# Kernel optimization log

Measured on AMD Instinct MI355X. Metric: run time of the kernel, lower is better.

## Reference

```python
import jax, jax.numpy as jnp
import numpy as np


def _gru(x, Wih, Whh, bih, bhh):
    # single-layer torch-style GRU; x: [B,T,D] -> [B,T,H]
    H = Whh.shape[1]
    gi_all = jnp.einsum('btd,gd->btg', x, Wih) + bih  # [B,T,3H], input gates precomputed

    def step(h, gi):
        gh = h @ Whh.T + bhh
        ir, iz, inn = jnp.split(gi, 3, axis=-1)
        hr, hz, hn = jnp.split(gh, 3, axis=-1)
        r = jax.nn.sigmoid(ir + hr)
        zg = jax.nn.sigmoid(iz + hz)
        n = jnp.tanh(inn + r * hn)
        h_new = (1.0 - zg) * n + zg * h
        return h_new, h_new

    h0 = jnp.zeros((x.shape[0], H), x.dtype)
    _, hs = jax.lax.scan(step, h0, jnp.swapaxes(gi_all, 0, 1))
    return jnp.swapaxes(hs, 0, 1)


def _post(h, W1, b1, W2, b2):
    h = jax.nn.leaky_relu(h @ W1.T + b1, 0.1)
    return jax.nn.leaky_relu(h @ W2.T + b2, 0.1)


def setup_inputs() -> dict:
    B, T, X, Z, H, L = 512, 100, 38, 3, 500, 20
    key = jax.random.key(0)
    ks = iter(jax.random.split(key, 40))
    r = lambda shape, s=0.05: jax.random.normal(next(ks), shape, jnp.float32) * s
    return {
        'x': jax.random.normal(next(ks), (B, T, X), jnp.float32),
        'eps': jax.random.normal(next(ks), (B, T, Z), jnp.float32),
        'enc_Wih': r((3 * H, X)), 'enc_Whh': r((3 * H, H)), 'enc_bih': r((3 * H,)), 'enc_bhh': r((3 * H,)),
        'enc_W1': r((H, H)), 'enc_b1': r((H,)), 'enc_W2': r((H, H)), 'enc_b2': r((H,)),
        'zm_W': r((Z, H + Z)), 'zm_b': r((Z,)), 'zs_W': r((Z, H + Z)), 'zs_b': r((Z,)),
        'flow_w': r((L, Z), 0.5), 'flow_b': r((L,), 0.5), 'flow_u': r((L, Z), 0.5),
        'dec_Wih': r((3 * H, Z)), 'dec_Whh': r((3 * H, H)), 'dec_bih': r((3 * H,)), 'dec_bhh': r((3 * H,)),
        'dec_W1': r((H, H)), 'dec_b1': r((H,)), 'dec_W2': r((H, H)), 'dec_b2': r((H,)),
        'xm_W': r((X, H)), 'xm_b': r((X,)), 'xs_W': r((X, H)), 'xs_b': r((X,)),
    }


def reference(x, eps, enc_Wih, enc_Whh, enc_bih, enc_bhh, enc_W1, enc_b1, enc_W2, enc_b2,
              zm_W, zm_b, zs_W, zs_b, flow_w, flow_b, flow_u,
              dec_Wih, dec_Whh, dec_bih, dec_bhh, dec_W1, dec_b1, dec_W2, dec_b2,
              xm_W, xm_b, xs_W, xs_b):
    # ---- Encoder ----
    h = _gru(x, enc_Wih, enc_Whh, enc_bih, enc_bhh)
    h = _post(h, enc_W1, enc_b1, enc_W2, enc_b2)

    def lat_step(z_prev, inputs):
        ht, et = inputs
        inp = jnp.concatenate([ht, z_prev], axis=-1)
        mu = inp @ zm_W.T + zm_b
        std = jax.nn.softplus(inp @ zs_W.T + zs_b) + 1e-4
        zt = mu + std * et
        return zt, (zt, mu, std)

    z0 = jnp.zeros((x.shape[0], zm_W.shape[0]), x.dtype)
    _, (z_gen, z_mu, z_std) = jax.lax.scan(
        lat_step, z0, (jnp.swapaxes(h, 0, 1), jnp.swapaxes(eps, 0, 1)))
    z_gen = jnp.swapaxes(z_gen, 0, 1)
    z_mu = jnp.swapaxes(z_mu, 0, 1)
    z_std = jnp.swapaxes(z_std, 0, 1)

    # ---- Planar flow stack ----
    def flow_step(carry, p):
        z, ld = carry
        w, b, u = p
        wu = jnp.sum(w * u)
        m = -1.0 + jax.nn.softplus(wu)
        u_hat = u + (m - wu) * w / (jnp.sum(w * w) + 1e-7)
        lin = jnp.sum(z * w, axis=-1, keepdims=True) + b  # [B,T,1]
        t = jnp.tanh(lin)
        fz = z + u_hat * t
        det = 1.0 + (1.0 - t * t) * jnp.sum(u_hat * w)  # sum(u_hat*psi)
        ld = ld + jnp.log(jnp.abs(det) + 1e-7)
        return (fz, ld), None

    ld0 = jnp.zeros(z_gen.shape[:-1] + (1,), z_gen.dtype)
    (z_fin, log_det_jac), _ = jax.lax.scan(flow_step, (z_gen, ld0), (flow_w, flow_b, flow_u))

    # ---- Decoder ----
    hd = _gru(z_fin, dec_Wih, dec_Whh, dec_bih, dec_bhh)
    hd = _post(hd, dec_W1, dec_b1, dec_W2, dec_b2)
    x_rec_mu = hd @ xm_W.T + xm_b
    x_rec_std = jax.nn.softplus(hd @ xs_W.T + xs_b) + 1e-4
    return (x_rec_mu, x_rec_std, z_gen, z_fin, z_mu, z_std, log_det_jac)
```

## Files before the change

### kernel.cpp

```cpp
#include <hip/hip_runtime.h>

typedef unsigned short u16;
typedef unsigned int u32;
typedef unsigned long long u64;
typedef __bf16 bf16x8 __attribute__((ext_vector_type(8)));
typedef float f32x4 __attribute__((ext_vector_type(4)));
typedef u16 u16x8 __attribute__((ext_vector_type(8)));
typedef u16 u16x4 __attribute__((ext_vector_type(4)));
typedef u32 u32x4 __attribute__((ext_vector_type(4)));

#define MFMA16x16(a,b,c) __builtin_amdgcn_mfma_f32_16x16x32_bf16((a),(b),(c),0,0,0)

static __device__ __forceinline__ u16 f2bf(float f){
  u32 u = __builtin_bit_cast(u32, f);
  u += 0x7fffu + ((u >> 16) & 1u);
  return (u16)(u >> 16);
}
static __device__ __forceinline__ float bf2f(u16 h){
  u32 u = ((u32)h) << 16;
  return __builtin_bit_cast(float, u);
}
static __device__ __forceinline__ float fast_sigmoid(float x){
  return 1.f / (1.f + __expf(-x));
}
static __device__ __forceinline__ float fast_tanh(float x){
  float e = __expf(2.f * x);
  return 1.f - 2.f / (e + 1.f);
}
static __device__ __forceinline__ float fast_softplus(float x){
  return (x > 15.f) ? x : __logf(1.f + __expf(x));
}
static __device__ __forceinline__ f32x4 zero4(){
  f32x4 v; v[0]=0.f; v[1]=0.f; v[2]=0.f; v[3]=0.f; return v;
}

static __device__ __forceinline__ void build_one(
    u16* __restrict__ dst, int mode, int NT, int idx,
    const float* __restrict__ W0, const float* __restrict__ b0,
    const float* __restrict__ W1, const float* __restrict__ b1)
{
  int j    = idx & 7;
  int lane = (idx >> 3) & 63;
  int ntks = idx >> 9;
  int nt   = ntks % NT;
  int ks   = ntks / NT;
  int k    = ks * 32 + ((lane >> 4) << 3) + j;
  int ncol = (nt << 4) + (lane & 15);
  float v = 0.f;
  if (mode == 0){
    int g = ncol >> 9;
    int jin = ncol & 511;
    if (jin < 500){
      int row = g * 500 + jin;
      if (k < 500) v = W0[row * 500 + k];
      else if (k == 511) v = b0[row];
    }
  } else if (mode == 2){
    if (ncol < 500){
      if (k < 500) v = W0[ncol * 500 + k];
      else if (k == 511) v = b0[ncol];
    }
  } else if (mode == 3){
    int c = ncol;
    if (c < 3){
      if (k < 500) v = W0[c * 503 + k];
      else if (k == 511) v = b0[c];
    } else if (c < 6){
      int cc = c - 3;
      if (k < 500) v = W1[cc * 503 + k];
      else if (k == 511) v = b1[cc];
    }
  } else if (mode == 4){
    int grp = ncol / 48;
    int cc  = ncol - grp * 48;
    if (grp < 2 && cc < 38){
      const float* W  = grp ? W1 : W0;
      const float* bb = grp ? b1 : b0;
      if (k < 500) v = W[cc * 500 + k];
      else if (k == 511) v = bb[cc];
    }
  } else {
    int g = ncol >> 9;
    int jin = ncol & 511;
    if (jin < 500 && k < 38) v = W0[(g * 500 + jin) * 38 + k];
  }
  dst[idx] = f2bf(v);
}

__global__ void build_all(
    u16* ENCF, u16* DECF, u16* EGIF, u16* PF0, u16* PF1, u16* PF2, u16* PF3,
    u16* ZFR, u16* HFR, float* FPP, u32* CNT,
    const float* enc_Whh, const float* enc_bhh, const float* enc_Wih,
    const float* dec_Whh, const float* dec_bhh,
    const float* enc_W1, const float* enc_b1, const float* enc_W2, const float* enc_b2,
    const float* dec_W1, const float* dec_b1, const float* dec_W2, const float* dec_b2,
    const float* zm_W, const float* zm_b, const float* zs_W, const float* zs_b,
    const float* xm_W, const float* xm_b, const float* xs_W, const float* xs_b,
    const float* flow_w, const float* flow_b, const float* flow_u)
{
  const int b = blockIdx.x, tid = threadIdx.x;
  if      (b < 3072)  build_one(ENCF,0,96,(b       )*256+tid, enc_Whh,enc_bhh,0,0);
  else if (b < 6144)  build_one(DECF,0,96,(b- 3072 )*256+tid, dec_Whh,dec_bhh,0,0);
  else if (b < 6528)  build_one(EGIF,5,96,(b- 6144 )*256+tid, enc_Wih,0,0,0);
  else if (b < 7552)  build_one(PF0 ,2,32,(b- 6528 )*256+tid, enc_W1,enc_b1,0,0);
  else if (b < 8576)  build_one(PF1 ,2,32,(b- 7552 )*256+tid, enc_W2,enc_b2,0,0);
  else if (b < 9600)  build_one(PF2 ,2,32,(b- 8576 )*256+tid, dec_W1,dec_b1,0,0);
  else if (b < 10624) build_one(PF3 ,2,32,(b- 9600 )*256+tid, dec_W2,dec_b2,0,0);
  else if (b < 10656) build_one(ZFR ,3, 1,(b-10624 )*256+tid, zm_W,zm_b,zs_W,zs_b);
  else if (b < 10848) build_one(HFR ,4, 6,(b-10656 )*256+tid, xm_W,xm_b,xs_W,xs_b);
  else if (b == 10848){
    if (tid < 20){
      int l = tid;
      float w0 = flow_w[l*3+0], w1 = flow_w[l*3+1], w2 = flow_w[l*3+2];
      float u0 = flow_u[l*3+0], u1 = flow_u[l*3+1], u2 = flow_u[l*3+2];
      float wu = w0*u0 + w1*u1 + w2*u2;
      float m  = -1.f + fast_softplus(wu);
      float ww = w0*w0 + w1*w1 + w2*w2 + 1e-7f;
      float sc = (m - wu) / ww;
      float uh0 = u0 + sc*w0, uh1 = u1 + sc*w1, uh2 = u2 + sc*w2;
      float uw  = uh0*w0 + uh1*w1 + uh2*w2;
      FPP[l*8+0]=w0; FPP[l*8+1]=w1; FPP[l*8+2]=w2; FPP[l*8+3]=flow_b[l];
      FPP[l*8+4]=uh0; FPP[l*8+5]=uh1; FPP[l*8+6]=uh2; FPP[l*8+7]=uw;
    }
  } else {
    for (int i = tid; i < 8192; i += 256) CNT[i] = 0;
  }
}

__global__ __launch_bounds__(512, 2) void gi_enc_kernel(
    const float* __restrict__ x, const u16* __restrict__ frag2,
    const float* __restrict__ bih, u16* __restrict__ gi)
{
  const int tid = threadIdx.x, lane = tid & 63, v = tid >> 6;
  const int q = lane >> 4, c = lane & 15;
  const size_t rowbase = (size_t)blockIdx.x * 32;
  u16 a[2][2][8];
  #pragma unroll
  for (int tile = 0; tile < 2; ++tile){
    const float* xr = x + (rowbase + tile*16 + c) * 38;
    #pragma unroll
    for (int j = 0; j < 8; ++j){
      int k0 = q*8 + j;
      a[tile][0][j] = f2bf(xr[k0]);
      int k1 = 32 + q*8 + j;
      a[tile][1][j] = (k1 < 38) ? f2bf(xr[k1]) : (u16)0;
    }
  }
  f32x4 acc[2][12];
  #pragma unroll
  for (int tile = 0; tile < 2; ++tile)
    #pragma unroll
    for (int i = 0; i < 12; ++i) acc[tile][i] = zero4();
  #pragma unroll
  for (int i = 0; i < 12; ++i){
    const int nt = v*12 + i;
    bf16x8 b0 = __builtin_bit_cast(bf16x8,
        *(const u16x8*)(frag2 + (((size_t)0*96 + nt)*64 + lane)*8));
    bf16x8 b1 = __builtin_bit_cast(bf16x8,
        *(const u16x8*)(frag2 + (((size_t)1*96 + nt)*64 + lane)*8));
    #pragma unroll
    for (int tile = 0; tile < 2; ++tile){
      bf16x8 a0 = __builtin_bit_cast(bf16x8, *(const u16x8*)a[tile][0]);
      bf16x8 a1 = __builtin_bit_cast(bf16x8, *(const u16x8*)a[tile][1]);
      acc[tile][i] = MFMA16x16(a0, b0, acc[tile][i]);
      acc[tile][i] = MFMA16x16(a1, b1, acc[tile][i]);
    }
  }
  #pragma unroll
  for (int i = 0; i < 12; ++i){
    const int nt = v*12 + i;
    const int ncol = nt*16 + c;
    const int g = ncol >> 9, jin = ncol & 511;
    const float bias = (jin < 500) ? bih[g*500 + jin] : 0.f;
    #pragma unroll
    for (int tile = 0; tile < 2; ++tile)
      #pragma unroll
      for (int r = 0; r < 4; ++r){
        size_t row = rowbase + tile*16 + q*4 + r;
        gi[row*1536 + ncol] = f2bf(acc[tile][i][r] + bias);
      }
  }
}

__global__ __launch_bounds__(256, 1) void gru8_kernel(
    const u16* __restrict__ frag, const u16* __restrict__ gix,
    const u64* __restrict__ zsrc, const float* __restrict__ Wih3,
    const float* __restrict__ bih3,
    u32* __restrict__ hbufbase, u16* __restrict__ hout, u32* __restrict__ cntbase)
{
  __shared__ u32 hstage[20800];
  const int tid  = threadIdx.x, lane = tid & 63;
  const int wv   = tid >> 6;
  const int q    = lane >> 4, c = lane & 15;
  const int gid  = blockIdx.x & 31, s = blockIdx.x >> 5;
  const int b0   = gid * 16;
  const int nt0  = s*4 + wv;
  const int col  = nt0*16 + c;
  u32* cnt = cntbase + gid * 128;
  u32* hb  = hbufbase + (size_t)gid * 8192;

  u16x8 wf[3][16];
  #pragma unroll
  for (int ks = 0; ks < 16; ++ks)
    #pragma unroll
    for (int g = 0; g < 3; ++g)
      wf[g][ks] = *(const u16x8*)(frag + (((size_t)ks*96 + g*32 + nt0)*64 + lane)*8);

  float wz[3][3] = {{0,0,0},{0,0,0},{0,0,0}}, wb[3] = {0,0,0};
  if (!gix && col < 500){
    #pragma unroll
    for (int g = 0; g < 3; ++g){
      #pragma unroll
      for (int k = 0; k < 3; ++k) wz[g][k] = Wih3[(g*500 + col)*3 + k];
      wb[g] = bih3[g*500 + col];
    }
  }

  const int srow = tid >> 4;
  const int spos = (tid & 15) * 2;

  float hold[4] = {0.f, 0.f, 0.f, 0.f};
  u16 giv[3][4];
  u64 zv[4];
  {
    u32 me = (col == 511) ? 0x3F80u : 0u;
    u32 pr = __shfl_xor(me, 1, 64);
    if (!(c & 1)){
      u32 val = me | (pr << 16);
      #pragma unroll
      for (int r = 0; r < 4; ++r){
        hstage[(q*4+r)*260 + (col>>1)] = val;
        __hip_atomic_store(hb + (q*4+r)*256 + (col>>1), val,
                           __ATOMIC_RELAXED, __HIP_MEMORY_SCOPE_AGENT);
      }
    }
    if (gix){
      #pragma unroll
      for (int g = 0; g < 3; ++g)
        #pragma unroll
        for (int r = 0; r < 4; ++r)
          giv[g][r] = __builtin_nontemporal_load(
              gix + ((size_t)(b0 + q*4 + r)*100 + 0)*1536 + g*512 + col);
    } else {
      #pragma unroll
      for (int r = 0; r < 4; ++r)
        zv[r] = zsrc[(size_t)(b0 + q*4 + r)*100 + 0];
    }
  }
  __syncthreads();
  if (tid == 0)
    __hip_atomic_fetch_add(cnt, 1u, __ATOMIC_RELAXED, __HIP_MEMORY_SCOPE_AGENT);

  #pragma unroll 1
  for (int t = 0; t < 100; ++t){
    if (tid == 0){
      const u32 target = 8u*(u32)(t+1);
      int guard = 0;
      while (__hip_atomic_load(cnt, __ATOMIC_RELAXED, __HIP_MEMORY_SCOPE_AGENT) < target){
        if (++guard > (1<<24)) break;
      }
    }
    __syncthreads();

    {
      const u64* src = (const u64*)(hb + (t & 1)*4096);
      u64 sv[7];
      #pragma unroll
      for (int r = 0; r < 7; ++r){
        const int rs = (s + 1 + r) & 7;
        sv[r] = __hip_atomic_load(src + srow*128 + rs*16 + (tid & 15),
                                  __ATOMIC_RELAXED, __HIP_MEMORY_SCOPE_AGENT);
      }
      #pragma unroll
      for (int r = 0; r < 7; ++r){
        const int rs = (s + 1 + r) & 7;
        *(u64*)&hstage[srow*260 + rs*32 + spos] = sv[r];
      }
    }
    __syncthreads();

    f32x4 acc0 = zero4(), acc1 = zero4(), acc2 = zero4();
    #pragma unroll
    for (int ks = 0; ks < 16; ++ks){
      bf16x8 af = *(const bf16x8*)&hstage[c*260 + ks*16 + q*4];
      acc0 = MFMA16x16(af, __builtin_bit_cast(bf16x8, wf[0][ks]), acc0);
      acc1 = MFMA16x16(af, __builtin_bit_cast(bf16x8, wf[1][ks]), acc1);
      acc2 = MFMA16x16(af, __builtin_bit_cast(bf16x8, wf[2][ks]), acc2);
    }
    __syncthreads();

    u16 hvv[4];
    u32* nxt = hb + ((t+1) & 1)*4096;
    {
      #pragma unroll
      for (int r = 0; r < 4; ++r){
        float gr, gz, gn;
        if (gix){
          gr = bf2f(giv[0][r]); gz = bf2f(giv[1][r]); gn = bf2f(giv[2][r]);
        } else {
          float z0 = bf2f((u16)(zv[r]));
          float z1 = bf2f((u16)(zv[r] >> 16));
          float z2 = bf2f((u16)(zv[r] >> 32));
          gr = z0*wz[0][0] + z1*wz[0][1] + z2*wz[0][2] + wb[0];
          gz = z0*wz[1][0] + z1*wz[1][1] + z2*wz[1][2] + wb[1];
          gn = z0*wz[2][0] + z1*wz[2][1] + z2*wz[2][2] + wb[2];
        }
        float ar = acc0[r] + gr;
        float az = acc1[r] + gz;
        float an = acc2[r];
        float rr = fast_sigmoid(ar);
        float zz = fast_sigmoid(az);
        float nn = fast_tanh(gn + rr*an);
        float h  = (1.f - zz)*nn + zz*hold[r];
        hold[r] = h;
        u16 hv16 = (col < 500) ? f2bf(h) : ((col == 511) ? (u16)0x3F80 : (u16)0);
        hvv[r] = hv16;
        u32 me = hv16;
        u32 pr = __shfl_xor(me, 1, 64);
        if (!(c & 1)){
          u32 val = me | (pr << 16);
          hstage[(q*4+r)*260 + (col>>1)] = val;
          __hip_atomic_store(nxt + (q*4+r)*256 + (col>>1), val,
                             __ATOMIC_RELAXED, __HIP_MEMORY_SCOPE_AGENT);
        }
      }
    }
    __syncthreads();
    if (tid == 0)
      __hip_atomic_fetch_add(cnt, 1u, __ATOMIC_RELAXED, __HIP_MEMORY_SCOPE_AGENT);
    #pragma unroll
    for (int r = 0; r < 4; ++r)
      __builtin_nontemporal_store(hvv[r],
          hout + ((size_t)(b0 + q*4 + r)*100 + t)*512 + col);
    if (t < 99){
      if (gix){
        #pragma unroll
        for (int g = 0; g < 3; ++g)
          #pragma unroll
          for (int r = 0; r < 4; ++r)
            giv[g][r] = __builtin_nontemporal_load(
                gix + ((size_t)(b0 + q*4 + r)*100 + (t+1))*1536 + g*512 + col);
      } else {
        #pragma unroll
        for (int r = 0; r < 4; ++r)
          zv[r] = zsrc[(size_t)(b0 + q*4 + r)*100 + (t+1)];
      }
    }
  }
}

__global__ __launch_bounds__(512, 4) void post_chain(
    const u16* __restrict__ A, const u16* __restrict__ fA,
    const u16* __restrict__ fB, const u16* __restrict__ f3,
    float* __restrict__ o0, float* __restrict__ o1, int mode)
{
  __shared__ u16 AS[32768];
  const int tid = threadIdx.x, lane = tid & 63, w = tid >> 6;
  const int q = lane >> 4, c = lane & 15;
  const int rt = w & 3, nh = w >> 2;
  const size_t rowbase = (size_t)blockIdx.x * 64;

  f32x4 acc[16];
  #pragma unroll
  for (int i = 0; i < 16; ++i) acc[i] = zero4();
  {
    const u16* Ar = A + (rowbase + rt*16 + c) * 512 + q * 8;
    #pragma unroll 1
    for (int ks = 0; ks < 16; ++ks){
      bf16x8 af = __builtin_bit_cast(bf16x8, *(const u16x8*)(Ar + ks * 32));
      #pragma unroll
      for (int i = 0; i < 16; ++i){
        const int nt = nh * 16 + i;
        bf16x8 bf = __builtin_bit_cast(bf16x8,
            *(const u16x8*)(fA + (((size_t)ks * 32 + nt) * 64 + lane) * 8));
        acc[i] = MFMA16x16(af, bf, acc[i]);
      }
    }
  }
  #pragma unroll
  for (int i = 0; i < 16; ++i){
    const int cl = (nh * 16 + i) * 16 + c;
    const int ks2 = cl >> 5, qq = (cl >> 3) & 3, j = cl & 7;
    #pragma unroll
    for (int r = 0; r < 4; ++r){
      const int m = q*4 + r;
      float v = acc[i][r];
      v = fmaxf(v, 0.1f * v);
      AS[(((rt*16 + ks2)*4 + qq)*16 + m)*8 + j] =
          (cl < 500) ? f2bf(v) : ((cl == 511) ? (u16)0x3F80 : (u16)0);
    }
  }
  __syncthreads();

  #pragma unroll
  for (int i = 0; i < 16; ++i) acc[i] = zero4();
  #pragma unroll 1
  for (int ks = 0; ks < 16; ++ks){
    bf16x8 af = __builtin_bit_cast(bf16x8,
        *(const u16x8*)&AS[(((rt*16 + ks)*4 + q)*16 + c)*8]);
    #pragma unroll
    for (int i = 0; i < 16; ++i){
      const int nt = nh * 16 + i;
      bf16x8 bf = __builtin_bit_cast(bf16x8,
          *(const u16x8*)(fB + (((size_t)ks * 32 + nt) * 64 + lane) * 8));
      acc[i] = MFMA16x16(af, bf, acc[i]);
    }
  }
  __syncthreads();
  #pragma unroll
  for (int i = 0; i < 16; ++i){
    const int cl = (nh * 16 + i) * 16 + c;
    const int ks2 = cl >> 5, qq = (cl >> 3) & 3, j = cl & 7;
    #pragma unroll
    for (int r = 0; r < 4; ++r){
      const int m = q*4 + r;
      float v = acc[i][r];
      v = fmaxf(v, 0.1f * v);
      AS[(((rt*16 + ks2)*4 + qq)*16 + m)*8 + j] =
          (cl < 500) ? f2bf(v) : ((cl == 511) ? (u16)0x3F80 : (u16)0);
    }
  }
  __syncthreads();

  if (mode == 0){
    if (w < 4){
      const int rt3 = w;
      f32x4 a3 = zero4();
      #pragma unroll 1
      for (int ks = 0; ks < 16; ++ks){
        bf16x8 af = __builtin_bit_cast(bf16x8,
            *(const u16x8*)&AS[(((rt3*16 + ks)*4 + q)*16 + c)*8]);
        bf16x8 bf = __builtin_bit_cast(bf16x8,
            *(const u16x8*)(f3 + (((size_t)ks * 64) + lane) * 8));
        a3 = MFMA16x16(af, bf, a3);
      }
      if (c < 6){
        #pragma unroll
        for (int r = 0; r < 4; ++r)
          o0[(rowbase + rt3*16 + q*4 + r)*8 + c] = a3[r];
      }
    }
  } else {
    const int rt3 = w & 3, hh = w >> 2;
    f32x4 a3[3];
    #pragma unroll
    for (int ii = 0; ii < 3; ++ii) a3[ii] = zero4();
    #pragma unroll 1
    for (int ks = 0; ks < 16; ++ks){
      bf16x8 af = __builtin_bit_cast(bf16x8,
          *(const u16x8*)&AS[(((rt3*16 + ks)*4 + q)*16 + c)*8]);
      #pragma unroll
      for (int ii = 0; ii < 3; ++ii){
        const int nt = hh*3 + ii;
        bf16x8 bf = __builtin_bit_cast(bf16x8,
            *(const u16x8*)(f3 + (((size_t)ks * 6 + nt) * 64 + lane) * 8));
        a3[ii] = MFMA16x16(af, bf, a3[ii]);
      }
    }
    #pragma unroll
    for (int ii = 0; ii < 3; ++ii){
      const int cc = (hh*3 + ii)*16 + c;
      const int grp = cc / 48;
      const int cl = cc - grp * 48;
      if (cl < 38){
        #pragma unroll
        for (int r = 0; r < 4; ++r){
          const size_t row = rowbase + rt3*16 + q*4 + r;
          if (grp == 0) o0[row*38 + cl] = a3[ii][r];
          else          o1[row*38 + cl] = fast_softplus(a3[ii][r]) + 1e-4f;
        }
      }
    }
  }
}

__global__ void scan_kernel(const float* __restrict__ hm, const float* __restrict__ eps,
                            const float* __restrict__ zmW, const float* __restrict__ zsW,
                            float* __restrict__ zgen, float* __restrict__ zmu,
                            float* __restrict__ zstd)
{
  int b = blockIdx.x * blockDim.x + threadIdx.x;
  if (b >= 512) return;
  float Wm[3][3], Ws[3][3];
  #pragma unroll
  for (int j = 0; j < 3; ++j)
    #pragma unroll
    for (int k = 0; k < 3; ++k){
      Wm[j][k] = zmW[j * 503 + 500 + k];
      Ws[j][k] = zsW[j * 503 + 500 + k];
    }
  float z0 = 0.f, z1 = 0.f, z2 = 0.f;
  for (int t = 0; t < 100; ++t){
    size_t row = (size_t)b * 100 + t;
    const float* h = hm + row * 8;
    const float* e = eps + row * 3;
    float zn[3];
    #pragma unroll
    for (int j = 0; j < 3; ++j){
      float m_ = h[j]     + Wm[j][0]*z0 + Wm[j][1]*z1 + Wm[j][2]*z2;
      float p_ = h[3 + j] + Ws[j][0]*z0 + Ws[j][1]*z1 + Ws[j][2]*z2;
      float s_ = fast_softplus(p_) + 1e-4f;
      float zv = m_ + s_ * e[j];
      zgen[row * 3 + j] = zv;
      zmu [row * 3 + j] = m_;
      zstd[row * 3 + j] = s_;
      zn[j] = zv;
    }
    z0 = zn[0]; z1 = zn[1]; z2 = zn[2];
  }
}

__global__ void flow_kernel(const float* __restrict__ zgen, const float* __restrict__ fp,
                            float* __restrict__ zfin, float* __restrict__ ldj,
                            u16* __restrict__ zf16)
{
  int idx = blockIdx.x * blockDim.x + threadIdx.x;
  if (idx >= 51200) return;
  float z0 = zgen[idx*3+0], z1 = zgen[idx*3+1], z2 = zgen[idx*3+2];
  float ld = 0.f;
  #pragma unroll 1
  for (int l = 0; l < 20; ++l){
    const float* p = fp + l * 8;
    float lin = z0*p[0] + z1*p[1] + z2*p[2] + p[3];
    float tt = fast_tanh(lin);
    z0 += p[4]*tt; z1 += p[5]*tt; z2 += p[6]*tt;
    float det = 1.f + (1.f - tt*tt) * p[7];
    ld += __logf(fabsf(det) + 1e-7f);
  }
  zfin[idx*3+0] = z0; zfin[idx*3+1] = z1; zfin[idx*3+2] = z2;
  ldj[idx] = ld;
  u16x4 o; o[0] = f2bf(z0); o[1] = f2bf(z1); o[2] = f2bf(z2); o[3] = 0x3F80;
  *(u16x4*)(zf16 + (size_t)idx * 4) = o;
}

extern "C" void kernel_launch(void* const* d_in, const int* in_sizes, int n_in,
                              void* d_out, int out_size, void* d_ws, size_t ws_size,
                              hipStream_t stream)
{
  const float* x       = (const float*)d_in[0];
  const float* eps     = (const float*)d_in[1];
  const float* enc_Wih = (const float*)d_in[2];
  const float* enc_Whh = (const float*)d_in[3];
  const float* enc_bih = (const float*)d_in[4];
  const float* enc_bhh = (const float*)d_in[5];
  const float* enc_W1  = (const float*)d_in[6];
  const float* enc_b1  = (const float*)d_in[7];
  const float* enc_W2  = (const float*)d_in[8];
  const float* enc_b2  = (const float*)d_in[9];
  const float* zm_W    = (const float*)d_in[10];
  const float* zm_b    = (const float*)d_in[11];
  const float* zs_W    = (const float*)d_in[12];
  const float* zs_b    = (const float*)d_in[13];
  const float* flow_w  = (const float*)d_in[14];
  const float* flow_b  = (const float*)d_in[15];
  const float* flow_u  = (const float*)d_in[16];
  const float* dec_Wih = (const float*)d_in[17];
  const float* dec_Whh = (const float*)d_in[18];
  const float* dec_bih = (const float*)d_in[19];
  const float* dec_bhh = (const float*)d_in[20];
  const float* dec_W1  = (const float*)d_in[21];
  const float* dec_b1  = (const float*)d_in[22];
  const float* dec_W2  = (const float*)d_in[23];
  const float* dec_b2  = (const float*)d_in[24];
  const float* xm_W    = (const float*)d_in[25];
  const float* xm_b    = (const float*)d_in[26];
  const float* xs_W    = (const float*)d_in[27];
  const float* xs_b    = (const float*)d_in[28];
  (void)in_sizes; (void)n_in; (void)out_size; (void)ws_size;

  float* out    = (float*)d_out;
  float* r_mu   = out;
  float* r_std  = out + 1945600;
  float* r_zgen = out + 3891200;
  float* r_zfin = out + 4044800;
  float* r_zmu  = out + 4198400;
  float* r_zstd = out + 4352000;
  float* r_ldj  = out + 4505600;

  char* ws = (char*)d_ws;
  size_t off = 0;
  auto alloc = [&](size_t bytes)->char*{
    char* p = ws + off;
    off += (bytes + 255) & ~(size_t)255;
    return p;
  };
  u16* H1    = (u16*)alloc((size_t)51200*512*2);
  u16* BIG   = (u16*)alloc((size_t)51200*1536*2);
  u16* ENCF  = (u16*)alloc((size_t)16*96*512*2);
  u16* DECF  = (u16*)alloc((size_t)16*96*512*2);
  u16* EGIF  = (u16*)alloc((size_t)2*96*512*2);
  u16* PF0   = (u16*)alloc((size_t)16*32*512*2);
  u16* PF1   = (u16*)alloc((size_t)16*32*512*2);
  u16* PF2   = (u16*)alloc((size_t)16*32*512*2);
  u16* PF3   = (u16*)alloc((size_t)16*32*512*2);
  u16* ZFR   = (u16*)alloc((size_t)16*1*512*2);
  u16* HFR   = (u16*)alloc((size_t)16*6*512*2);
  float* FPP = (float*)alloc((size_t)20*8*4);
  float* HM  = (float*)alloc((size_t)51200*8*4);
  u16* ZF16  = (u16*)alloc((size_t)51200*4*2);
  u32* HBUF  = (u32*)alloc((size_t)32*2*16*512*2);
  u32* CNT   = (u32*)alloc((size_t)2*32*128*4);

  build_all<<<10850,256,0,stream>>>(ENCF,DECF,EGIF,PF0,PF1,PF2,PF3,ZFR,HFR,FPP,CNT,
      enc_Whh,enc_bhh,enc_Wih,dec_Whh,dec_bhh,
      enc_W1,enc_b1,enc_W2,enc_b2,dec_W1,dec_b1,dec_W2,dec_b2,
      zm_W,zm_b,zs_W,zs_b,xm_W,xm_b,xs_W,xs_b,flow_w,flow_b,flow_u);

  gi_enc_kernel<<<1600,512,0,stream>>>(x, EGIF, enc_bih, BIG);
  gru8_kernel<<<256,256,0,stream>>>(ENCF, BIG, nullptr, nullptr, nullptr,
                                    HBUF, H1, CNT);
  post_chain<<<800,512,0,stream>>>(H1, PF0, PF1, ZFR, HM, nullptr, 0);

  scan_kernel<<<2,256,0,stream>>>(HM, eps, zm_W, zs_W, r_zgen, r_zmu, r_zstd);
  flow_kernel<<<200,256,0,stream>>>(r_zgen, FPP, r_zfin, r_ldj, ZF16);

  gru8_kernel<<<256,256,0,stream>>>(DECF, nullptr, (const u64*)ZF16,
                                    dec_Wih, dec_bih, HBUF, H1, CNT + 32*128);
  post_chain<<<800,512,0,stream>>>(H1, PF2, PF3, HFR, r_mu, r_std, 1);
}
```

Before: 1.203 ms.

## Replace counter barrier in GRU recurrence with per-word step tags on hidden-state exchange

The 8-block cooperative GRU used to synchronise each timestep with an atomic counter: thread 0 spun on it, then a block barrier, then every block incremented it after a second barrier. Now each 64-bit hidden-state word carries a 16-bit timestep tag next to three bf16 values. Readers poll their own words until the tags match, which removes the counter, the spin by thread 0 and one __syncthreads per step. In exchange the exchange buffer is larger and unpacking into shared memory is more complex, and correctness depends on the tagged words being zeroed first and on the reused decoder buffer having tags that do not collide with the encoder's.

```diff
diff --git a/kernel.cpp b/kernel.cpp
--- a/kernel.cpp
+++ b/kernel.cpp
@@ -89,7 +89,7 @@
 
 __global__ void build_all(
     u16* ENCF, u16* DECF, u16* EGIF, u16* PF0, u16* PF1, u16* PF2, u16* PF3,
-    u16* ZFR, u16* HFR, float* FPP, u32* CNT,
+    u16* ZFR, u16* HFR, float* FPP, u32* HBZ,
     const float* enc_Whh, const float* enc_bhh, const float* enc_Wih,
     const float* dec_Whh, const float* dec_bhh,
     const float* enc_W1, const float* enc_b1, const float* enc_W2, const float* enc_b2,
@@ -123,7 +123,9 @@
       FPP[l*8+4]=uh0; FPP[l*8+5]=uh1; FPP[l*8+6]=uh2; FPP[l*8+7]=uw;
     }
   } else {
-    for (int i = tid; i < 8192; i += 256) CNT[i] = 0;
+    const int zb = b - 10849;
+    u32* p = HBZ + (size_t)zb * 3072;
+    for (int i = tid; i < 3072; i += 256) p[i] = 0;
   }
 }
 
@@ -186,9 +188,10 @@
     const u16* __restrict__ frag, const u16* __restrict__ gix,
     const u64* __restrict__ zsrc, const float* __restrict__ Wih3,
     const float* __restrict__ bih3,
-    u32* __restrict__ hbufbase, u16* __restrict__ hout, u32* __restrict__ cntbase)
+    u64* __restrict__ hbufbase, u16* __restrict__ hout)
 {
   __shared__ u32 hstage[20800];
+  u16* hs16 = (u16*)hstage;
   const int tid  = threadIdx.x, lane = tid & 63;
   const int wv   = tid >> 6;
   const int q    = lane >> 4, c = lane & 15;
@@ -196,8 +199,8 @@
   const int b0   = gid * 16;
   const int nt0  = s*4 + wv;
   const int col  = nt0*16 + c;
-  u32* cnt = cntbase + gid * 128;
-  u32* hb  = hbufbase + (size_t)gid * 8192;
+  const int cm3  = c % 3, cd3 = c / 3;
+  u64* hb = hbufbase + (size_t)gid * 6144;
 
   u16x8 wf[3][16];
   #pragma unroll
@@ -216,23 +219,47 @@
     }
   }
 
-  const int srow = tid >> 4;
-  const int spos = (tid & 15) * 2;
+  const int prow = tid >> 4, pi = tid & 15;
+  u32 goff[11], laddr[11];
+  u32 vmask = 0, trimask = 0, emask = 0;
+  #pragma unroll
+  for (int k = 0; k < 11; ++k){
+    const int e = pi + 16*k;
+    if (e < 168){
+      const int sidx = e / 24, sub = e - sidx*24;
+      const int srk  = (s + 1 + sidx) & 7;
+      const int tile = sub / 6, j = sub - tile*6;
+      goff[k]  = (u32)((prow*8 + srk)*24 + sub);
+      laddr[k] = (u32)(prow*520 + srk*64 + tile*16 + 3*j);
+      vmask |= 1u << k;
+      if (j < 5){
+        trimask |= 1u << k;
+        if (!(j & 1)) emask |= 1u << k;
+      }
+    } else { goff[k] = 0; laddr[k] = 0; }
+  }
 
   float hold[4] = {0.f, 0.f, 0.f, 0.f};
   u16 giv[3][4];
   u64 zv[4];
   {
-    u32 me = (col == 511) ? 0x3F80u : 0u;
-    u32 pr = __shfl_xor(me, 1, 64);
+    u16 h0 = (col == 511) ? (u16)0x3F80 : (u16)0;
+    u32 me = h0;
+    u32 pr = (u32)__shfl_xor((int)me, 1, 64);
     if (!(c & 1)){
       u32 val = me | (pr << 16);
       #pragma unroll
-      for (int r = 0; r < 4; ++r){
+      for (int r = 0; r < 4; ++r)
         hstage[(q*4+r)*260 + (col>>1)] = val;
-        __hip_atomic_store(hb + (q*4+r)*256 + (col>>1), val,
+    }
+    u32 nb1 = (u32)__shfl((int)me, lane+1, 64);
+    u32 nb2 = (u32)__shfl((int)me, lane+2, 64);
+    if (cm3 == 0){
+      u64 val = 1ull | ((u64)me << 16) | ((u64)nb1 << 32) | ((u64)nb2 << 48);
+      #pragma unroll
+      for (int r = 0; r < 4; ++r)
+        __hip_atomic_store(hb + (size_t)(((q*4+r)*8 + s)*24 + wv*6 + cd3), val,
                            __ATOMIC_RELAXED, __HIP_MEMORY_SCOPE_AGENT);
-      }
     }
     if (gix){
       #pragma unroll
@@ -247,34 +274,45 @@
         zv[r] = zsrc[(size_t)(b0 + q*4 + r)*100 + 0];
     }
   }
-  __syncthreads();
-  if (tid == 0)
-    __hip_atomic_fetch_add(cnt, 1u, __ATOMIC_RELAXED, __HIP_MEMORY_SCOPE_AGENT);
 
   #pragma unroll 1
   for (int t = 0; t < 100; ++t){
-    if (tid == 0){
-      const u32 target = 8u*(u32)(t+1);
+    {
+      const u64* src = hb + (size_t)(t & 1) * 3072;
+      const u32 want = (u32)(t + 1);
+      u64 v[11];
+      #pragma unroll
+      for (int k = 0; k < 11; ++k)
+        if (vmask >> k & 1)
+          v[k] = __hip_atomic_load(src + goff[k],
+                                   __ATOMIC_RELAXED, __HIP_MEMORY_SCOPE_AGENT);
       int guard = 0;
-      while (__hip_atomic_load(cnt, __ATOMIC_RELAXED, __HIP_MEMORY_SCOPE_AGENT) < target){
-        if (++guard > (1<<24)) break;
-      }
-    }
-    __syncthreads();
-
-    {
-      const u64* src = (const u64*)(hb + (t & 1)*4096);
-      u64 sv[7];
-      #pragma unroll
-      for (int r = 0; r < 7; ++r){
-        const int rs = (s + 1 + r) & 7;
-        sv[r] = __hip_atomic_load(src + srow*128 + rs*16 + (tid & 15),
-                                  __ATOMIC_RELAXED, __HIP_MEMORY_SCOPE_AGENT);
-      }
-      #pragma unroll
-      for (int r = 0; r < 7; ++r){
-        const int rs = (s + 1 + r) & 7;
-        *(u64*)&hstage[srow*260 + rs*32 + spos] = sv[r];
+      while (true){
+        u32 bad = 0;
+        #pragma unroll
+        for (int k = 0; k < 11; ++k)
+          if ((vmask >> k & 1) && (u32)(u16)v[k] != want) bad |= 1u << k;
+        if (!bad || ++guard > (1<<16)) break;
+        #pragma unroll
+        for (int k = 0; k < 11; ++k)
+          if (bad >> k & 1)
+            v[k] = __hip_atomic_load(src + goff[k],
+                                     __ATOMIC_RELAXED, __HIP_MEMORY_SCOPE_AGENT);
+      }
+      #pragma unroll
+      for (int k = 0; k < 11; ++k){
+        if (!(vmask >> k & 1)) continue;
+        if (trimask >> k & 1){
+          if (emask >> k & 1){
+            hstage[laddr[k] >> 1] = (u32)(v[k] >> 16);
+            hs16[laddr[k] + 2]    = (u16)(v[k] >> 48);
+          } else {
+            hs16[laddr[k]]              = (u16)(v[k] >> 16);
+            hstage[(laddr[k] + 1) >> 1] = (u32)(v[k] >> 32);
+          }
+        } else {
+          hs16[laddr[k]] = (u16)(v[k] >> 16);
+        }
       }
     }
     __syncthreads();
@@ -290,44 +328,43 @@
     __syncthreads();
 
     u16 hvv[4];
-    u32* nxt = hb + ((t+1) & 1)*4096;
-    {
-      #pragma unroll
-      for (int r = 0; r < 4; ++r){
-        float gr, gz, gn;
-        if (gix){
-          gr = bf2f(giv[0][r]); gz = bf2f(giv[1][r]); gn = bf2f(giv[2][r]);
-        } else {
-          float z0 = bf2f((u16)(zv[r]));
-          float z1 = bf2f((u16)(zv[r] >> 16));
-          float z2 = bf2f((u16)(zv[r] >> 32));
-          gr = z0*wz[0][0] + z1*wz[0][1] + z2*wz[0][2] + wb[0];
-          gz = z0*wz[1][0] + z1*wz[1][1] + z2*wz[1][2] + wb[1];
-          gn = z0*wz[2][0] + z1*wz[2][1] + z2*wz[2][2] + wb[2];
-        }
-        float ar = acc0[r] + gr;
-        float az = acc1[r] + gz;
-        float an = acc2[r];
-        float rr = fast_sigmoid(ar);
-        float zz = fast_sigmoid(az);
-        float nn = fast_tanh(gn + rr*an);
-        float h  = (1.f - zz)*nn + zz*hold[r];
-        hold[r] = h;
-        u16 hv16 = (col < 500) ? f2bf(h) : ((col == 511) ? (u16)0x3F80 : (u16)0);
-        hvv[r] = hv16;
-        u32 me = hv16;
-        u32 pr = __shfl_xor(me, 1, 64);
-        if (!(c & 1)){
-          u32 val = me | (pr << 16);
-          hstage[(q*4+r)*260 + (col>>1)] = val;
-          __hip_atomic_store(nxt + (q*4+r)*256 + (col>>1), val,
-                             __ATOMIC_RELAXED, __HIP_MEMORY_SCOPE_AGENT);
-        }
-      }
-    }
-    __syncthreads();
-    if (tid == 0)
-      __hip_atomic_fetch_add(cnt, 1u, __ATOMIC_RELAXED, __HIP_MEMORY_SCOPE_AGENT);
+    u64* nxt = hb + (size_t)((t+1) & 1) * 3072;
+    const u64 tag = (u64)(t + 2);
+    #pragma unroll
+    for (int r = 0; r < 4; ++r){
+      float gr, gz, gn;
+      if (gix){
+        gr = bf2f(giv[0][r]); gz = bf2f(giv[1][r]); gn = bf2f(giv[2][r]);
+      } else {
+        float z0 = bf2f((u16)(zv[r]));
+        float z1 = bf2f((u16)(zv[r] >> 16));
+        float z2 = bf2f((u16)(zv[r] >> 32));
+        gr = z0*wz[0][0] + z1*wz[0][1] + z2*wz[0][2] + wb[0];
+        gz = z0*wz[1][0] + z1*wz[1][1] + z2*wz[1][2] + wb[1];
+        gn = z0*wz[2][0] + z1*wz[2][1] + z2*wz[2][2] + wb[2];
+      }
+      float ar = acc0[r] + gr;
+      float az = acc1[r] + gz;
+      float an = acc2[r];
+      float rr = fast_sigmoid(ar);
+      float zz = fast_sigmoid(az);
+      float nn = fast_tanh(gn + rr*an);
+      float h  = (1.f - zz)*nn + zz*hold[r];
+      hold[r] = h;
+      u16 hv16 = (col < 500) ? f2bf(h) : ((col == 511) ? (u16)0x3F80 : (u16)0);
+      hvv[r] = hv16;
+      u32 me = hv16;
+      u32 pr = (u32)__shfl_xor((int)me, 1, 64);
+      if (!(c & 1))
+        hstage[(q*4+r)*260 + (col>>1)] = me | (pr << 16);
+      u32 nb1 = (u32)__shfl((int)me, lane+1, 64);
+      u32 nb2 = (u32)__shfl((int)me, lane+2, 64);
+      if (cm3 == 0){
+        u64 val = tag | ((u64)me << 16) | ((u64)nb1 << 32) | ((u64)nb2 << 48);
+        __hip_atomic_store(nxt + (size_t)(((q*4+r)*8 + s)*24 + wv*6 + cd3), val,
+                           __ATOMIC_RELAXED, __HIP_MEMORY_SCOPE_AGENT);
+      }
+    }
     #pragma unroll
     for (int r = 0; r < 4; ++r)
       __builtin_nontemporal_store(hvv[r],
@@ -598,23 +635,23 @@
   float* FPP = (float*)alloc((size_t)20*8*4);
   float* HM  = (float*)alloc((size_t)51200*8*4);
   u16* ZF16  = (u16*)alloc((size_t)51200*4*2);
-  u32* HBUF  = (u32*)alloc((size_t)32*2*16*512*2);
-  u32* CNT   = (u32*)alloc((size_t)2*32*128*4);
-
-  build_all<<<10850,256,0,stream>>>(ENCF,DECF,EGIF,PF0,PF1,PF2,PF3,ZFR,HFR,FPP,CNT,
+  u64* HBUF  = (u64*)alloc((size_t)32*6144*8);
+
+  build_all<<<10977,256,0,stream>>>(ENCF,DECF,EGIF,PF0,PF1,PF2,PF3,ZFR,HFR,FPP,
+      (u32*)HBUF,
       enc_Whh,enc_bhh,enc_Wih,dec_Whh,dec_bhh,
       enc_W1,enc_b1,enc_W2,enc_b2,dec_W1,dec_b1,dec_W2,dec_b2,
       zm_W,zm_b,zs_W,zs_b,xm_W,xm_b,xs_W,xs_b,flow_w,flow_b,flow_u);
 
   gi_enc_kernel<<<1600,512,0,stream>>>(x, EGIF, enc_bih, BIG);
   gru8_kernel<<<256,256,0,stream>>>(ENCF, BIG, nullptr, nullptr, nullptr,
-                                    HBUF, H1, CNT);
+                                    HBUF, H1);
   post_chain<<<800,512,0,stream>>>(H1, PF0, PF1, ZFR, HM, nullptr, 0);
 
   scan_kernel<<<2,256,0,stream>>>(HM, eps, zm_W, zs_W, r_zgen, r_zmu, r_zstd);
   flow_kernel<<<200,256,0,stream>>>(r_zgen, FPP, r_zfin, r_ldj, ZF16);
 
   gru8_kernel<<<256,256,0,stream>>>(DECF, nullptr, (const u64*)ZF16,
-                                    dec_Wih, dec_bih, HBUF, H1, CNT + 32*128);
+                                    dec_Wih, dec_bih, HBUF, H1);
   post_chain<<<800,512,0,stream>>>(H1, PF2, PF3, HFR, r_mu, r_std, 1);
 }
```

After: 1.434 ms. 19.2% more time.

## Replace counter barrier in GRU scan with tagged per-element hidden-state flags

Applied to the files above, without the earlier changes.

The cross-block GRU recurrence no longer uses a shared atomic counter that every block increments and polls with two __syncthreads per step. Each hidden-state pair is now written as a 64-bit word carrying a step tag, and each thread polls only the words it needs until the tags match. This removes the global barrier round trip and lets consumers start as soon as their own data arrives. The cost is doubled exchange-buffer traffic, a larger zeroing pass in the build kernel, and reliance on tag ordering with a bounded spin.

```diff
diff --git a/kernel.cpp b/kernel.cpp
--- a/kernel.cpp
+++ b/kernel.cpp
@@ -89,7 +89,7 @@
 
 __global__ void build_all(
     u16* ENCF, u16* DECF, u16* EGIF, u16* PF0, u16* PF1, u16* PF2, u16* PF3,
-    u16* ZFR, u16* HFR, float* FPP, u32* CNT,
+    u16* ZFR, u16* HFR, float* FPP, u32* HBZ,
     const float* enc_Whh, const float* enc_bhh, const float* enc_Wih,
     const float* dec_Whh, const float* dec_bhh,
     const float* enc_W1, const float* enc_b1, const float* enc_W2, const float* enc_b2,
@@ -123,7 +123,9 @@
       FPP[l*8+4]=uh0; FPP[l*8+5]=uh1; FPP[l*8+6]=uh2; FPP[l*8+7]=uw;
     }
   } else {
-    for (int i = tid; i < 8192; i += 256) CNT[i] = 0;
+    const int zb = b - 10849;
+    u32* p = HBZ + (size_t)zb * 4096;
+    for (int i = tid; i < 4096; i += 256) p[i] = 0;
   }
 }
 
@@ -186,7 +188,7 @@
     const u16* __restrict__ frag, const u16* __restrict__ gix,
     const u64* __restrict__ zsrc, const float* __restrict__ Wih3,
     const float* __restrict__ bih3,
-    u32* __restrict__ hbufbase, u16* __restrict__ hout, u32* __restrict__ cntbase)
+    u64* __restrict__ hbufbase, u16* __restrict__ hout, int tagbase)
 {
   __shared__ u32 hstage[20800];
   const int tid  = threadIdx.x, lane = tid & 63;
@@ -196,8 +198,7 @@
   const int b0   = gid * 16;
   const int nt0  = s*4 + wv;
   const int col  = nt0*16 + c;
-  u32* cnt = cntbase + gid * 128;
-  u32* hb  = hbufbase + (size_t)gid * 8192;
+  u64* hb = hbufbase + (size_t)gid * 8192;
 
   u16x8 wf[3][16];
   #pragma unroll
@@ -216,22 +217,32 @@
     }
   }
 
-  const int srow = tid >> 4;
-  const int spos = (tid & 15) * 2;
+  const int prow = tid >> 4, pi = tid & 15;
+  u32 goff[14];
+  #pragma unroll
+  for (int k = 0; k < 14; ++k){
+    const int e = pi + 16*k;
+    const int sidx = e >> 5, sub = e & 31;
+    const int srk  = (s + 1 + sidx) & 7;
+    goff[k] = (u32)(((prow*8 + srk) << 5) + sub);
+  }
+  const int kp = (pi % 7)*2 + (pi >= 7 ? 1 : 0);
 
   float hold[4] = {0.f, 0.f, 0.f, 0.f};
   u16 giv[3][4];
   u64 zv[4];
   {
-    u32 me = (col == 511) ? 0x3F80u : 0u;
-    u32 pr = __shfl_xor(me, 1, 64);
+    u16 h0 = (col == 511) ? (u16)0x3F80 : (u16)0;
+    u32 me = h0;
+    u32 pr = (u32)__shfl_xor((int)me, 1, 64);
     if (!(c & 1)){
-      u32 val = me | (pr << 16);
+      u32 pairval = me | (pr << 16);
+      u64 val = ((u64)(u32)(tagbase + 1) << 32) | pairval;
       #pragma unroll
       for (int r = 0; r < 4; ++r){
-        hstage[(q*4+r)*260 + (col>>1)] = val;
-        __hip_atomic_store(hb + (q*4+r)*256 + (col>>1), val,
-                           __ATOMIC_RELAXED, __HIP_MEMORY_SCOPE_AGENT);
+        hstage[(q*4+r)*260 + (col>>1)] = pairval;
+        __hip_atomic_store(hb + ((size_t)((q*4+r)*8 + s) << 5) + wv*8 + (c>>1),
+                           val, __ATOMIC_RELAXED, __HIP_MEMORY_SCOPE_AGENT);
       }
     }
     if (gix){
@@ -247,34 +258,51 @@
         zv[r] = zsrc[(size_t)(b0 + q*4 + r)*100 + 0];
     }
   }
-  __syncthreads();
-  if (tid == 0)
-    __hip_atomic_fetch_add(cnt, 1u, __ATOMIC_RELAXED, __HIP_MEMORY_SCOPE_AGENT);
 
   #pragma unroll 1
   for (int t = 0; t < 100; ++t){
-    if (tid == 0){
-      const u32 target = 8u*(u32)(t+1);
-      int guard = 0;
-      while (__hip_atomic_load(cnt, __ATOMIC_RELAXED, __HIP_MEMORY_SCOPE_AGENT) < target){
-        if (++guard > (1<<24)) break;
-      }
-    }
-    __syncthreads();
-
     {
-      const u64* src = (const u64*)(hb + (t & 1)*4096);
-      u64 sv[7];
-      #pragma unroll
-      for (int r = 0; r < 7; ++r){
-        const int rs = (s + 1 + r) & 7;
-        sv[r] = __hip_atomic_load(src + srow*128 + rs*16 + (tid & 15),
-                                  __ATOMIC_RELAXED, __HIP_MEMORY_SCOPE_AGENT);
-      }
-      #pragma unroll
-      for (int r = 0; r < 7; ++r){
-        const int rs = (s + 1 + r) & 7;
-        *(u64*)&hstage[srow*260 + rs*32 + spos] = sv[r];
+      const u64* src = hb + (size_t)(t & 1) * 4096;
+      const u32 want = (u32)(tagbase + t + 1);
+      u64 v[14];
+      {
+        u64 pv; int rounds = 0;
+        for (;;){
+          pv = __hip_atomic_load(src + goff[kp],
+                                 __ATOMIC_RELAXED, __HIP_MEMORY_SCOPE_AGENT);
+          if ((u32)(pv >> 32) == want) break;
+          if (++rounds > 4096) break;
+          __builtin_amdgcn_s_sleep(1);
+        }
+        v[kp] = pv;
+      }
+      #pragma unroll
+      for (int k = 0; k < 14; ++k)
+        if (k != kp)
+          v[k] = __hip_atomic_load(src + goff[k],
+                                   __ATOMIC_RELAXED, __HIP_MEMORY_SCOPE_AGENT);
+      {
+        int rounds = 0;
+        for (;;){
+          u32 bad = 0;
+          #pragma unroll
+          for (int k = 0; k < 14; ++k)
+            if ((u32)(v[k] >> 32) != want) bad |= 1u << k;
+          if (!bad || ++rounds > 4096) break;
+          __builtin_amdgcn_s_sleep(1);
+          #pragma unroll
+          for (int k = 0; k < 14; ++k)
+            if (bad >> k & 1)
+              v[k] = __hip_atomic_load(src + goff[k],
+                                       __ATOMIC_RELAXED, __HIP_MEMORY_SCOPE_AGENT);
+        }
+      }
+      #pragma unroll
+      for (int k = 0; k < 14; ++k){
+        const int e = pi + 16*k;
+        const int sidx = e >> 5, sub = e & 31;
+        const int srk  = (s + 1 + sidx) & 7;
+        hstage[prow*260 + srk*32 + sub] = (u32)v[k];
       }
     }
     __syncthreads();
@@ -290,44 +318,41 @@
     __syncthreads();
 
     u16 hvv[4];
-    u32* nxt = hb + ((t+1) & 1)*4096;
-    {
-      #pragma unroll
-      for (int r = 0; r < 4; ++r){
-        float gr, gz, gn;
-        if (gix){
-          gr = bf2f(giv[0][r]); gz = bf2f(giv[1][r]); gn = bf2f(giv[2][r]);
-        } else {
-          float z0 = bf2f((u16)(zv[r]));
-          float z1 = bf2f((u16)(zv[r] >> 16));
-          float z2 = bf2f((u16)(zv[r] >> 32));
-          gr = z0*wz[0][0] + z1*wz[0][1] + z2*wz[0][2] + wb[0];
-          gz = z0*wz[1][0] + z1*wz[1][1] + z2*wz[1][2] + wb[1];
-          gn = z0*wz[2][0] + z1*wz[2][1] + z2*wz[2][2] + wb[2];
-        }
-        float ar = acc0[r] + gr;
-        float az = acc1[r] + gz;
-        float an = acc2[r];
-        float rr = fast_sigmoid(ar);
-        float zz = fast_sigmoid(az);
-        float nn = fast_tanh(gn + rr*an);
-        float h  = (1.f - zz)*nn + zz*hold[r];
-        hold[r] = h;
-        u16 hv16 = (col < 500) ? f2bf(h) : ((col == 511) ? (u16)0x3F80 : (u16)0);
-        hvv[r] = hv16;
-        u32 me = hv16;
-        u32 pr = __shfl_xor(me, 1, 64);
-        if (!(c & 1)){
-          u32 val = me | (pr << 16);
-          hstage[(q*4+r)*260 + (col>>1)] = val;
-          __hip_atomic_store(nxt + (q*4+r)*256 + (col>>1), val,
-                             __ATOMIC_RELAXED, __HIP_MEMORY_SCOPE_AGENT);
-        }
-      }
-    }
-    __syncthreads();
-    if (tid == 0)
-      __hip_atomic_fetch_add(cnt, 1u, __ATOMIC_RELAXED, __HIP_MEMORY_SCOPE_AGENT);
+    u64* nxt = hb + (size_t)((t+1) & 1) * 4096;
+    const u64 taghi = ((u64)(u32)(tagbase + t + 2)) << 32;
+    #pragma unroll
+    for (int r = 0; r < 4; ++r){
+      float gr, gz, gn;
+      if (gix){
+        gr = bf2f(giv[0][r]); gz = bf2f(giv[1][r]); gn = bf2f(giv[2][r]);
+      } else {
+        float z0 = bf2f((u16)(zv[r]));
+        float z1 = bf2f((u16)(zv[r] >> 16));
+        float z2 = bf2f((u16)(zv[r] >> 32));
+        gr = z0*wz[0][0] + z1*wz[0][1] + z2*wz[0][2] + wb[0];
+        gz = z0*wz[1][0] + z1*wz[1][1] + z2*wz[1][2] + wb[1];
+        gn = z0*wz[2][0] + z1*wz[2][1] + z2*wz[2][2] + wb[2];
+      }
+      float ar = acc0[r] + gr;
+      float az = acc1[r] + gz;
+      float an = acc2[r];
+      float rr = fast_sigmoid(ar);
+      float zz = fast_sigmoid(az);
+      float nn = fast_tanh(gn + rr*an);
+      float h  = (1.f - zz)*nn + zz*hold[r];
+      hold[r] = h;
+      u16 hv16 = (col < 500) ? f2bf(h) : ((col == 511) ? (u16)0x3F80 : (u16)0);
+      hvv[r] = hv16;
+      u32 me = hv16;
+      u32 pr = (u32)__shfl_xor((int)me, 1, 64);
+      if (!(c & 1)){
+        u32 pairval = me | (pr << 16);
+        hstage[(q*4+r)*260 + (col>>1)] = pairval;
+        __hip_atomic_store(nxt + ((size_t)((q*4+r)*8 + s) << 5) + wv*8 + (c>>1),
+                           taghi | pairval,
+                           __ATOMIC_RELAXED, __HIP_MEMORY_SCOPE_AGENT);
+      }
+    }
     #pragma unroll
     for (int r = 0; r < 4; ++r)
       __builtin_nontemporal_store(hvv[r],
@@ -598,23 +623,23 @@
   float* FPP = (float*)alloc((size_t)20*8*4);
   float* HM  = (float*)alloc((size_t)51200*8*4);
   u16* ZF16  = (u16*)alloc((size_t)51200*4*2);
-  u32* HBUF  = (u32*)alloc((size_t)32*2*16*512*2);
-  u32* CNT   = (u32*)alloc((size_t)2*32*128*4);
-
-  build_all<<<10850,256,0,stream>>>(ENCF,DECF,EGIF,PF0,PF1,PF2,PF3,ZFR,HFR,FPP,CNT,
+  u64* HBUF  = (u64*)alloc((size_t)32*8192*8);
+
+  build_all<<<10977,256,0,stream>>>(ENCF,DECF,EGIF,PF0,PF1,PF2,PF3,ZFR,HFR,FPP,
+      (u32*)HBUF,
       enc_Whh,enc_bhh,enc_Wih,dec_Whh,dec_bhh,
       enc_W1,enc_b1,enc_W2,enc_b2,dec_W1,dec_b1,dec_W2,dec_b2,
       zm_W,zm_b,zs_W,zs_b,xm_W,xm_b,xs_W,xs_b,flow_w,flow_b,flow_u);
 
   gi_enc_kernel<<<1600,512,0,stream>>>(x, EGIF, enc_bih, BIG);
   gru8_kernel<<<256,256,0,stream>>>(ENCF, BIG, nullptr, nullptr, nullptr,
-                                    HBUF, H1, CNT);
+                                    HBUF, H1, 0);
   post_chain<<<800,512,0,stream>>>(H1, PF0, PF1, ZFR, HM, nullptr, 0);
 
   scan_kernel<<<2,256,0,stream>>>(HM, eps, zm_W, zs_W, r_zgen, r_zmu, r_zstd);
   flow_kernel<<<200,256,0,stream>>>(r_zgen, FPP, r_zfin, r_ldj, ZF16);
 
   gru8_kernel<<<256,256,0,stream>>>(DECF, nullptr, (const u64*)ZF16,
-                                    dec_Wih, dec_bih, HBUF, H1, CNT + 32*128);
+                                    dec_Wih, dec_bih, HBUF, H1, 128);
   post_chain<<<800,512,0,stream>>>(H1, PF2, PF3, HFR, r_mu, r_std, 1);
 }
```

Measured after the change: 1.359 ms. +13.0%, slower.
